# Performance work log

Hardware: AMD Instinct MI355X
Metric: run time of the kernel (lower is better)

The kernel has to match this reference:

```python
import jax, jax.numpy as jnp
import numpy as np

D_MODEL = 1024
NHEAD = 16
HEAD_DIM = D_MODEL // NHEAD


def setup_inputs() -> dict:
    key = jax.random.key(0)
    ks = jax.random.split(key, 11)
    B, S = 2, 2048
    s = 1.0 / np.sqrt(D_MODEL)
    return {
        "query": jax.random.normal(ks[0], (B, S, D_MODEL), jnp.float32),
        "key": jax.random.normal(ks[1], (B, S, D_MODEL), jnp.float32),
        "value": jax.random.normal(ks[2], (B, S, D_MODEL), jnp.float32),
        "wq_w": jax.random.normal(ks[3], (D_MODEL, D_MODEL), jnp.float32) * s,
        "wq_b": jax.random.normal(ks[4], (D_MODEL,), jnp.float32) * s,
        "wk_w": jax.random.normal(ks[5], (D_MODEL, D_MODEL), jnp.float32) * s,
        "wk_b": jax.random.normal(ks[6], (D_MODEL,), jnp.float32) * s,
        "wv_w": jax.random.normal(ks[7], (D_MODEL, D_MODEL), jnp.float32) * s,
        "wv_b": jax.random.normal(ks[8], (D_MODEL,), jnp.float32) * s,
        "wo_w": jax.random.normal(ks[9], (D_MODEL, D_MODEL), jnp.float32) * s,
        "wo_b": jax.random.normal(ks[10], (D_MODEL,), jnp.float32) * s,
    }


def reference(query, key, value, wq_w, wq_b, wk_w, wk_b, wv_w, wv_b, wo_w, wo_b):
    B, S, _ = query.shape
    # torch Linear: x @ W.T + b
    def proj(x, w, b):
        y = x @ w.T + b
        return y.reshape(B, S, NHEAD, HEAD_DIM).transpose(0, 2, 1, 3)  # [B,H,S,Dh]

    Q = proj(query, wq_w, wq_b)
    K = proj(key, wk_w, wk_b)
    V = proj(value, wv_w, wv_b)

    scale = 1.0 / np.sqrt(HEAD_DIM).astype(np.float32)
    scores = jnp.einsum("bhqd,bhkd->bhqk", Q, K) * scale  # [B,H,S,S]
    causal = jnp.tril(jnp.ones((S, S), dtype=bool))
    scores = jnp.where(causal, scores, -jnp.inf)
    attn = jax.nn.softmax(scores, axis=-1)
    out = jnp.einsum("bhqk,bhkd->bhqd", attn, V)  # [B,H,S,Dh]
    out = out.transpose(0, 2, 1, 3).reshape(B, S, D_MODEL)
    return out @ wo_w.T + wo_b
```

## Files before the change

### kernel.cpp

```cpp
#include <hip/hip_runtime.h>
#include <stdint.h>

#define D_MODEL 1024
#define S_LEN   2048
#define NHEAD   16
#define HEAD_DIM 64
#define BATCH   2
#define M_TOT   (BATCH * S_LEN)
#define Q_SCALE 0.18033688011112042f

using bf16x8 = __attribute__((ext_vector_type(8))) short;
using f32x4  = __attribute__((ext_vector_type(4))) float;

__device__ __forceinline__ unsigned short f2bf(float f) {
  union { float f; unsigned int u; } v; v.f = f;
  unsigned int u = v.u;
  return (unsigned short)((u + 0x7FFFu + ((u >> 16) & 1u)) >> 16);
}
__device__ __forceinline__ unsigned int pkbf(float a, float b) {
#if __has_builtin(__builtin_amdgcn_cvt_pk_bf16_f32)
  auto p = __builtin_amdgcn_cvt_pk_bf16_f32(a, b);
  union { decltype(p) v; unsigned int u; } c; c.v = p;
  return c.u;
#else
  return (unsigned int)f2bf(a) | ((unsigned int)f2bf(b) << 16);
#endif
}
__device__ __forceinline__ bf16x8 cvt8(const float* p) {
  const float4 a = *(const float4*)p;
  const float4 b = *(const float4*)(p + 4);
  union { unsigned int u[4]; bf16x8 v; } r;
  r.u[0] = pkbf(a.x, a.y); r.u[1] = pkbf(a.z, a.w);
  r.u[2] = pkbf(b.x, b.y); r.u[3] = pkbf(b.z, b.w);
  return r.v;
}
__device__ __forceinline__ float fexp2(float x) {
#if __has_builtin(__builtin_amdgcn_exp2f)
  return __builtin_amdgcn_exp2f(x);
#else
  return __expf(x * 0.69314718055994531f);
#endif
}
__device__ __forceinline__ void async16(const unsigned short* g, short* l) {
  __builtin_amdgcn_global_load_lds(
      reinterpret_cast<const __attribute__((address_space(1))) unsigned int*>(
          reinterpret_cast<uintptr_t>(g)),
      reinterpret_cast<__attribute__((address_space(3))) unsigned int*>(
          reinterpret_cast<uintptr_t>(l)),
      16, 0, 0);
}

#define LDK 40

__global__ __launch_bounds__(256)
void cast_all(const float* __restrict__ wq, const float* __restrict__ wk,
              const float* __restrict__ wv, const float* __restrict__ wo,
              const float* __restrict__ q, const float* __restrict__ k,
              const float* __restrict__ v,
              unsigned short* __restrict__ wb,
              unsigned short* __restrict__ qb, unsigned short* __restrict__ kb,
              unsigned short* __restrict__ vb)
{
  const int z = blockIdx.y;
  const float* src;
  unsigned short* d;
  size_t n;
  switch (z) {
    case 0: src = wq; d = wb;                                   n = (size_t)D_MODEL * D_MODEL; break;
    case 1: src = wk; d = wb + (size_t)1 * D_MODEL * D_MODEL;   n = (size_t)D_MODEL * D_MODEL; break;
    case 2: src = wv; d = wb + (size_t)2 * D_MODEL * D_MODEL;   n = (size_t)D_MODEL * D_MODEL; break;
    case 3: src = wo; d = wb + (size_t)3 * D_MODEL * D_MODEL;   n = (size_t)D_MODEL * D_MODEL; break;
    case 4: src = q;  d = qb;                                   n = (size_t)M_TOT * D_MODEL;   break;
    case 5: src = k;  d = kb;                                   n = (size_t)M_TOT * D_MODEL;   break;
    default: src = v; d = vb;                                   n = (size_t)M_TOT * D_MODEL;   break;
  }
  const size_t i = ((size_t)blockIdx.x * 256 + threadIdx.x) * 8;
  if (i < n) *(bf16x8*)(d + i) = cvt8(src + i);
}

__device__ __forceinline__ void gemm_tile_lds(const unsigned short* __restrict__ A,
                                              const unsigned short* __restrict__ W,
                                              int m0, int n0,
                                              short* As, short* Bs,
                                              f32x4 acc[4][4])
{
  const int t    = threadIdx.x;
  const int lane = t & 63;
  const int w    = t >> 6;
  const int quad = lane >> 4;
  const int l16  = lane & 15;
  const int wm   = (w >> 1) * 64;
  const int wn   = (w & 1) * 64;
  const int srow = w * 16 + (lane >> 2);
  const int scol = (lane & 3) * 8;

  for (int mt = 0; mt < 4; ++mt)
    for (int nt = 0; nt < 4; ++nt)
      acc[mt][nt] = f32x4{0.f, 0.f, 0.f, 0.f};

  for (int kt = 0; kt < D_MODEL / 32; ++kt) {
    const int kc = kt * 32 + scol;
    __syncthreads();
    async16(A + (size_t)(m0 + srow)      * D_MODEL + kc, As + srow * 32 + scol);
    async16(A + (size_t)(m0 + 64 + srow) * D_MODEL + kc, As + (64 + srow) * 32 + scol);
    async16(W + (size_t)(n0 + srow)      * D_MODEL + kc, Bs + srow * 32 + scol);
    async16(W + (size_t)(n0 + 64 + srow) * D_MODEL + kc, Bs + (64 + srow) * 32 + scol);
    __syncthreads();

    bf16x8 af[4], bfr[4];
    for (int mt = 0; mt < 4; ++mt)
      af[mt] = *(const bf16x8*)(As + (wm + mt * 16 + l16) * 32 + quad * 8);
    for (int nt = 0; nt < 4; ++nt)
      bfr[nt] = *(const bf16x8*)(Bs + (wn + nt * 16 + l16) * 32 + quad * 8);
    for (int mt = 0; mt < 4; ++mt)
      for (int nt = 0; nt < 4; ++nt)
        acc[mt][nt] = __builtin_amdgcn_mfma_f32_16x16x32_bf16(af[mt], bfr[nt], acc[mt][nt], 0, 0, 0);
  }
}

__device__ __forceinline__ void gemm_tile_f32(const float* __restrict__ A,
                                              const unsigned short* __restrict__ W,
                                              int m0, int n0,
                                              short* As, short* Bs,
                                              f32x4 acc[4][4])
{
  const int t    = threadIdx.x;
  const int lane = t & 63;
  const int w    = t >> 6;
  const int quad = lane >> 4;
  const int l16  = lane & 15;
  const int wm   = (w >> 1) * 64;
  const int wn   = (w & 1) * 64;
  const int srow = t >> 2;
  const int scol = (t & 3) * 8;

  for (int mt = 0; mt < 4; ++mt)
    for (int nt = 0; nt < 4; ++nt)
      acc[mt][nt] = f32x4{0.f, 0.f, 0.f, 0.f};

  for (int kt = 0; kt < D_MODEL / 32; ++kt) {
    const int kc = kt * 32 + scol;
    const bf16x8 a0 = cvt8(A + (size_t)(m0 + srow)      * D_MODEL + kc);
    const bf16x8 a1 = cvt8(A + (size_t)(m0 + srow + 64) * D_MODEL + kc);
    const bf16x8 b0 = *(const bf16x8*)(W + (size_t)(n0 + srow)      * D_MODEL + kc);
    const bf16x8 b1 = *(const bf16x8*)(W + (size_t)(n0 + srow + 64) * D_MODEL + kc);
    __syncthreads();
    *(bf16x8*)(As + (srow)      * LDK + scol) = a0;
    *(bf16x8*)(As + (srow + 64) * LDK + scol) = a1;
    *(bf16x8*)(Bs + (srow)      * LDK + scol) = b0;
    *(bf16x8*)(Bs + (srow + 64) * LDK + scol) = b1;
    __syncthreads();

    bf16x8 af[4], bfr[4];
    for (int mt = 0; mt < 4; ++mt)
      af[mt] = *(const bf16x8*)(As + (wm + mt * 16 + l16) * LDK + quad * 8);
    for (int nt = 0; nt < 4; ++nt)
      bfr[nt] = *(const bf16x8*)(Bs + (wn + nt * 16 + l16) * LDK + quad * 8);
    for (int mt = 0; mt < 4; ++mt)
      for (int nt = 0; nt < 4; ++nt)
        acc[mt][nt] = __builtin_amdgcn_mfma_f32_16x16x32_bf16(af[mt], bfr[nt], acc[mt][nt], 0, 0, 0);
  }
}

__device__ __forceinline__ void qkv_epilogue(int z, int m0, int n0,
                                             const float* __restrict__ bias,
                                             float scale,
                                             unsigned short* __restrict__ dst,
                                             f32x4 acc[4][4])
{
  const int t    = threadIdx.x;
  const int lane = t & 63;
  const int w    = t >> 6;
  const int quad = lane >> 4;
  const int l16  = lane & 15;
  const int wm   = (w >> 1) * 64;
  const int wn   = (w & 1) * 64;

  for (int nt = 0; nt < 4; ++nt) {
    const int n = n0 + wn + nt * 16 + l16;
    const float bb = bias[n];
    const int h = n >> 6, d = n & 63;
    for (int mt = 0; mt < 4; ++mt) {
      for (int r = 0; r < 4; ++r) {
        const int m = m0 + wm + mt * 16 + quad * 4 + r;
        const int b = m >> 11, s = m & 2047;
        const unsigned short val = f2bf((acc[mt][nt][r] + bb) * scale);
        if (z < 2)
          dst[((size_t)((b * NHEAD + h) * S_LEN + s)) * HEAD_DIM + d] = val;
        else
          dst[((size_t)((b * NHEAD + h) * HEAD_DIM + d)) * S_LEN + s] = val;
      }
    }
  }
}

__global__ __launch_bounds__(256)
void qkv_fast(const unsigned short* __restrict__ qb,
              const unsigned short* __restrict__ kb,
              const unsigned short* __restrict__ vb,
              const unsigned short* __restrict__ wqb,
              const unsigned short* __restrict__ wkb,
              const unsigned short* __restrict__ wvb,
              const float* __restrict__ bq, const float* __restrict__ bk,
              const float* __restrict__ bv,
              unsigned short* __restrict__ Qh, unsigned short* __restrict__ Kh,
              unsigned short* __restrict__ VhT)
{
  __shared__ __attribute__((aligned(16))) short As[128 * 32];
  __shared__ __attribute__((aligned(16))) short Bs[128 * 32];
  const int z = blockIdx.z;
  const unsigned short* A    = (z == 0) ? qb  : (z == 1) ? kb  : vb;
  const unsigned short* W    = (z == 0) ? wqb : (z == 1) ? wkb : wvb;
  const float*          bias = (z == 0) ? bq  : (z == 1) ? bk  : bv;
  unsigned short*       dst  = (z == 0) ? Qh  : (z == 1) ? Kh  : VhT;
  const float           scale = (z == 0) ? Q_SCALE : 1.0f;

  const int m0 = blockIdx.x * 128, n0 = blockIdx.y * 128;
  f32x4 acc[4][4];
  gemm_tile_lds(A, W, m0, n0, As, Bs, acc);
  qkv_epilogue(z, m0, n0, bias, scale, dst, acc);
}

__global__ __launch_bounds__(256)
void qkv_slow(const float* __restrict__ query, const float* __restrict__ key,
              const float* __restrict__ value,
              const unsigned short* __restrict__ wqb,
              const unsigned short* __restrict__ wkb,
              const unsigned short* __restrict__ wvb,
              const float* __restrict__ bq, const float* __restrict__ bk,
              const float* __restrict__ bv,
              unsigned short* __restrict__ Qh, unsigned short* __restrict__ Kh,
              unsigned short* __restrict__ VhT)
{
  __shared__ __attribute__((aligned(16))) short As[128 * LDK];
  __shared__ __attribute__((aligned(16))) short Bs[128 * LDK];
  const int z = blockIdx.z;
  const float*          A    = (z == 0) ? query : (z == 1) ? key : value;
  const unsigned short* W    = (z == 0) ? wqb   : (z == 1) ? wkb : wvb;
  const float*          bias = (z == 0) ? bq    : (z == 1) ? bk  : bv;
  unsigned short*       dst  = (z == 0) ? Qh    : (z == 1) ? Kh  : VhT;
  const float           scale = (z == 0) ? Q_SCALE : 1.0f;

  const int m0 = blockIdx.x * 128, n0 = blockIdx.y * 128;
  f32x4 acc[4][4];
  gemm_tile_f32(A, W, m0, n0, As, Bs, acc);
  qkv_epilogue(z, m0, n0, bias, scale, dst, acc);
}

__global__ __launch_bounds__(256)
void out_proj(const unsigned short* __restrict__ Oh,
              const unsigned short* __restrict__ wob,
              const float* __restrict__ bo,
              float* __restrict__ dst)
{
  __shared__ __attribute__((aligned(16))) short As[128 * 32];
  __shared__ __attribute__((aligned(16))) short Bs[128 * 32];
  const int m0 = blockIdx.x * 128, n0 = blockIdx.y * 128;
  f32x4 acc[4][4];
  gemm_tile_lds(Oh, wob, m0, n0, As, Bs, acc);

  const int t    = threadIdx.x;
  const int lane = t & 63;
  const int w    = t >> 6;
  const int quad = lane >> 4;
  const int l16  = lane & 15;
  const int wm   = (w >> 1) * 64;
  const int wn   = (w & 1) * 64;

  for (int nt = 0; nt < 4; ++nt) {
    const int n = n0 + wn + nt * 16 + l16;
    const float bb = bo[n];
    for (int mt = 0; mt < 4; ++mt)
      for (int r = 0; r < 4; ++r) {
        const int m = m0 + wm + mt * 16 + quad * 4 + r;
        dst[(size_t)m * D_MODEL + n] = acc[mt][nt][r] + bb;
      }
  }
}

__global__ __launch_bounds__(256)
void attn_kernel(const unsigned short* __restrict__ Qh,
                 const unsigned short* __restrict__ Kh,
                 const unsigned short* __restrict__ VhT,
                 unsigned short* __restrict__ O)
{
  __shared__ __attribute__((aligned(16))) short Ks[128 * 72];
  __shared__ __attribute__((aligned(16))) short Vts[64 * 136];
  __shared__ __attribute__((aligned(16))) short Ps[4][16 * 136];

  const int bh   = blockIdx.x;
  const int qt   = (int)gridDim.y - 1 - (int)blockIdx.y;
  const int q0   = qt * 64;
  const int b    = bh >> 4;
  const int h    = bh & 15;
  const int t    = threadIdx.x;
  const int w    = t >> 6;
  const int lane = t & 63;
  const int quad = lane >> 4;
  const int l16  = lane & 15;
  const size_t headK = (size_t)bh * S_LEN * HEAD_DIM;
  const size_t headV = (size_t)bh * HEAD_DIM * S_LEN;

  bf16x8 qf[2];
  {
    const size_t qrow = (size_t)bh * S_LEN + (q0 + w * 16 + l16);
    qf[0] = *(const bf16x8*)(Qh + qrow * HEAD_DIM + quad * 8);
    qf[1] = *(const bf16x8*)(Qh + qrow * HEAD_DIM + 32 + quad * 8);
  }
  bf16x8 ones;
  for (int j = 0; j < 8; ++j) ones[j] = (short)0x3F80;

  f32x4 lacc = f32x4{0.f, 0.f, 0.f, 0.f};
  f32x4 oacc[4];
  for (int dt = 0; dt < 4; ++dt) oacc[dt] = f32x4{0.f, 0.f, 0.f, 0.f};

  const int rowbase = q0 + w * 16;
  const int rowmax  = rowbase + 15;
  const int kr = t >> 3, kc = (t & 7) * 8;
  const int vd = t >> 4, vc = (t & 15) * 8;

  const int nkt = (qt + 2) >> 1;
  for (int kt = 0; kt < nkt; ++kt) {
    const int k0 = kt * 128;
    __syncthreads();
    for (int i = 0; i < 4; ++i) {
      const int rr = kr + i * 32;
      *(bf16x8*)(Ks + rr * 72 + kc) =
          *(const bf16x8*)(Kh + headK + (size_t)(k0 + rr) * HEAD_DIM + kc);
      const int dd = vd + i * 16;
      *(bf16x8*)(Vts + dd * 136 + vc) =
          *(const bf16x8*)(VhT + headV + (size_t)dd * S_LEN + k0 + vc);
    }
    __syncthreads();

    float st[8][4];
    for (int nt = 0; nt < 8; ++nt) {
      const int c0 = k0 + nt * 16;
      if (c0 <= rowmax) {
        f32x4 s = f32x4{0.f, 0.f, 0.f, 0.f};
        for (int ks = 0; ks < 2; ++ks) {
          const bf16x8 kf = *(const bf16x8*)(Ks + (nt * 16 + l16) * 72 + ks * 32 + quad * 8);
          s = __builtin_amdgcn_mfma_f32_16x16x32_bf16(qf[ks], kf, s, 0, 0, 0);
        }
        if (c0 + 15 <= rowbase) {
          for (int r = 0; r < 4; ++r) st[nt][r] = fexp2(s[r]);
        } else {
          const int colg = c0 + l16;
          for (int r = 0; r < 4; ++r) {
            const int rowg = rowbase + quad * 4 + r;
            st[nt][r] = (colg <= rowg) ? fexp2(s[r]) : 0.f;
          }
        }
      } else {
        for (int r = 0; r < 4; ++r) st[nt][r] = 0.f;
      }
    }
    for (int nt = 0; nt < 8; nt += 2) {
      for (int r = 0; r < 4; ++r) {
        const unsigned int u = pkbf(st[nt][r], st[nt + 1][r]);
        short* base = &Ps[w][(quad * 4 + r) * 136 + nt * 16 + l16];
        base[0]  = (short)(u & 0xffffu);
        base[16] = (short)(u >> 16);
      }
    }

    for (int ks = 0; ks < 4; ++ks) {
      if (k0 + ks * 32 > rowmax) break;
      const bf16x8 pf = *(const bf16x8*)(&Ps[w][0] + l16 * 136 + ks * 32 + quad * 8);
      lacc = __builtin_amdgcn_mfma_f32_16x16x32_bf16(pf, ones, lacc, 0, 0, 0);
      for (int dt = 0; dt < 4; ++dt) {
        const bf16x8 vf = *(const bf16x8*)(Vts + (dt * 16 + l16) * 136 + ks * 32 + quad * 8);
        oacc[dt] = __builtin_amdgcn_mfma_f32_16x16x32_bf16(pf, vf, oacc[dt], 0, 0, 0);
      }
    }
  }

  for (int dt = 0; dt < 4; ++dt) {
    for (int r = 0; r < 4; ++r) {
      const int rowg = q0 + w * 16 + quad * 4 + r;
      O[(size_t)(b * S_LEN + rowg) * D_MODEL + h * 64 + dt * 16 + l16] =
          f2bf(oacc[dt][r] / lacc[r]);
    }
  }
}

extern "C" void kernel_launch(void* const* d_in, const int* in_sizes, int n_in,
                              void* d_out, int out_size, void* d_ws, size_t ws_size,
                              hipStream_t stream)
{
  (void)in_sizes; (void)n_in; (void)out_size;
  const float* q  = (const float*)d_in[0];
  const float* k  = (const float*)d_in[1];
  const float* v  = (const float*)d_in[2];
  const float* wq = (const float*)d_in[3];
  const float* bq = (const float*)d_in[4];
  const float* wk = (const float*)d_in[5];
  const float* bk = (const float*)d_in[6];
  const float* wv = (const float*)d_in[7];
  const float* bv = (const float*)d_in[8];
  const float* wo = (const float*)d_in[9];
  const float* bo = (const float*)d_in[10];
  float* out = (float*)d_out;

  unsigned short* wb  = (unsigned short*)d_ws;
  unsigned short* wqb = wb;
  unsigned short* wkb = wb + (size_t)1 * D_MODEL * D_MODEL;
  unsigned short* wvb = wb + (size_t)2 * D_MODEL * D_MODEL;
  unsigned short* wob = wb + (size_t)3 * D_MODEL * D_MODEL;
  unsigned short* Kh  = wb + (size_t)4 * D_MODEL * D_MODEL;
  unsigned short* VhT = Kh + (size_t)M_TOT * D_MODEL;
  unsigned short* Oh  = VhT + (size_t)M_TOT * D_MODEL;
  unsigned short* qb  = Oh;
  unsigned short* vb  = Oh + (size_t)M_TOT * D_MODEL;
  unsigned short* Qh  = (unsigned short*)d_out;
  unsigned short* kb  = Qh + (size_t)M_TOT * D_MODEL;

  const bool fast = ws_size >= (size_t)40 * 1024 * 1024;

  dim3 g1(M_TOT / 128, D_MODEL / 128, 3);
  if (fast) {
    dim3 gc((size_t)M_TOT * D_MODEL / (256 * 8), 7, 1);
    cast_all<<<gc, 256, 0, stream>>>(wq, wk, wv, wo, q, k, v, wb, qb, kb, vb);
    qkv_fast<<<g1, 256, 0, stream>>>(qb, kb, vb, wqb, wkb, wvb, bq, bk, bv, Qh, Kh, VhT);
  } else {
    dim3 gc((size_t)D_MODEL * D_MODEL / (256 * 8), 4, 1);
    cast_all<<<gc, 256, 0, stream>>>(wq, wk, wv, wo, q, k, v, wb, qb, kb, vb);
    qkv_slow<<<g1, 256, 0, stream>>>(q, k, v, wqb, wkb, wvb, bq, bk, bv, Qh, Kh, VhT);
  }

  dim3 g2(BATCH * NHEAD, S_LEN / 64, 1);
  attn_kernel<<<g2, 256, 0, stream>>>(Qh, Kh, VhT, Oh);

  dim3 g3(M_TOT / 128, D_MODEL / 128, 1);
  out_proj<<<g3, 256, 0, stream>>>(Oh, wob, bo, out);
}
```

Measured before the change: 223.5 us.

## Keep attention probabilities in registers via transposed QK^T and permlane swaps

```diff
diff --git a/kernel.cpp b/kernel.cpp
--- a/kernel.cpp
+++ b/kernel.cpp
@@ -48,6 +48,33 @@
       reinterpret_cast<__attribute__((address_space(3))) unsigned int*>(
           reinterpret_cast<uintptr_t>(l)),
       16, 0, 0);
+}
+
+__device__ __forceinline__ void swap32(unsigned int& x, unsigned int& y) {
+#if __has_builtin(__builtin_amdgcn_permlane32_swap)
+  auto r = __builtin_amdgcn_permlane32_swap(x, y, false, false);
+  x = (unsigned int)r[0]; y = (unsigned int)r[1];
+#else
+  const int lane = threadIdx.x & 63;
+  unsigned int sx = (unsigned int)__shfl_xor((int)x, 32);
+  unsigned int sy = (unsigned int)__shfl_xor((int)y, 32);
+  unsigned int nx = (lane & 32) ? sy : x;
+  unsigned int ny = (lane & 32) ? y : sx;
+  x = nx; y = ny;
+#endif
+}
+__device__ __forceinline__ void swap16(unsigned int& x, unsigned int& y) {
+#if __has_builtin(__builtin_amdgcn_permlane16_swap)
+  auto r = __builtin_amdgcn_permlane16_swap(x, y, false, false);
+  x = (unsigned int)r[0]; y = (unsigned int)r[1];
+#else
+  const int lane = threadIdx.x & 63;
+  unsigned int sx = (unsigned int)__shfl_xor((int)x, 16);
+  unsigned int sy = (unsigned int)__shfl_xor((int)y, 16);
+  unsigned int nx = (lane & 16) ? sy : x;
+  unsigned int ny = (lane & 16) ? y : sx;
+  x = nx; y = ny;
+#endif
 }
 
 #define LDK 40
@@ -257,7 +284,7 @@
   __shared__ __attribute__((aligned(16))) short Bs[128 * 32];
   const int m0 = blockIdx.x * 128, n0 = blockIdx.y * 128;
   f32x4 acc[4][4];
-  gemm_tile_lds(Oh, wob, m0, n0, As, Bs, acc);
+  gemm_tile_lds(Oh, wob, bo ? m0 : m0, n0, As, Bs, acc);
 
   const int t    = threadIdx.x;
   const int lane = t & 63;
@@ -286,7 +313,6 @@
 {
   __shared__ __attribute__((aligned(16))) short Ks[128 * 72];
   __shared__ __attribute__((aligned(16))) short Vts[64 * 136];
-  __shared__ __attribute__((aligned(16))) short Ps[4][16 * 136];
 
   const int bh   = blockIdx.x;
   const int qt   = (int)gridDim.y - 1 - (int)blockIdx.y;
@@ -316,6 +342,7 @@
 
   const int rowbase = q0 + w * 16;
   const int rowmax  = rowbase + 15;
+  const int qg      = rowbase + l16;
   const int kr = t >> 3, kc = (t & 7) * 8;
   const int vd = t >> 4, vc = (t & 15) * 8;
 
@@ -334,43 +361,48 @@
     __syncthreads();
 
     float st[8][4];
+#pragma unroll
     for (int nt = 0; nt < 8; ++nt) {
       const int c0 = k0 + nt * 16;
       if (c0 <= rowmax) {
         f32x4 s = f32x4{0.f, 0.f, 0.f, 0.f};
+#pragma unroll
         for (int ks = 0; ks < 2; ++ks) {
           const bf16x8 kf = *(const bf16x8*)(Ks + (nt * 16 + l16) * 72 + ks * 32 + quad * 8);
-          s = __builtin_amdgcn_mfma_f32_16x16x32_bf16(qf[ks], kf, s, 0, 0, 0);
+          s = __builtin_amdgcn_mfma_f32_16x16x32_bf16(kf, qf[ks], s, 0, 0, 0);
         }
         if (c0 + 15 <= rowbase) {
+#pragma unroll
           for (int r = 0; r < 4; ++r) st[nt][r] = fexp2(s[r]);
         } else {
-          const int colg = c0 + l16;
-          for (int r = 0; r < 4; ++r) {
-            const int rowg = rowbase + quad * 4 + r;
-            st[nt][r] = (colg <= rowg) ? fexp2(s[r]) : 0.f;
-          }
+          const int kgb = c0 + quad * 4;
+#pragma unroll
+          for (int r = 0; r < 4; ++r)
+            st[nt][r] = (kgb + r <= qg) ? fexp2(s[r]) : 0.f;
         }
       } else {
+#pragma unroll
         for (int r = 0; r < 4; ++r) st[nt][r] = 0.f;
       }
     }
-    for (int nt = 0; nt < 8; nt += 2) {
-      for (int r = 0; r < 4; ++r) {
-        const unsigned int u = pkbf(st[nt][r], st[nt + 1][r]);
-        short* base = &Ps[w][(quad * 4 + r) * 136 + nt * 16 + l16];
-        base[0]  = (short)(u & 0xffffu);
-        base[16] = (short)(u >> 16);
-      }
-    }
-
+
+#pragma unroll
     for (int ks = 0; ks < 4; ++ks) {
-      if (k0 + ks * 32 > rowmax) break;
-      const bf16x8 pf = *(const bf16x8*)(&Ps[w][0] + l16 * 136 + ks * 32 + quad * 8);
-      lacc = __builtin_amdgcn_mfma_f32_16x16x32_bf16(pf, ones, lacc, 0, 0, 0);
-      for (int dt = 0; dt < 4; ++dt) {
-        const bf16x8 vf = *(const bf16x8*)(Vts + (dt * 16 + l16) * 136 + ks * 32 + quad * 8);
-        oacc[dt] = __builtin_amdgcn_mfma_f32_16x16x32_bf16(pf, vf, oacc[dt], 0, 0, 0);
+      if (k0 + ks * 32 <= rowmax) {
+        unsigned int pa = pkbf(st[2 * ks][0],     st[2 * ks][1]);
+        unsigned int pb = pkbf(st[2 * ks][2],     st[2 * ks][3]);
+        unsigned int pc = pkbf(st[2 * ks + 1][0], st[2 * ks + 1][1]);
+        unsigned int pe = pkbf(st[2 * ks + 1][2], st[2 * ks + 1][3]);
+        swap32(pa, pc); swap32(pb, pe);
+        swap16(pa, pc); swap16(pb, pe);
+        union { unsigned int u[4]; bf16x8 v; } pf;
+        pf.u[0] = pa; pf.u[1] = pb; pf.u[2] = pc; pf.u[3] = pe;
+        lacc = __builtin_amdgcn_mfma_f32_16x16x32_bf16(pf.v, ones, lacc, 0, 0, 0);
+#pragma unroll
+        for (int dt = 0; dt < 4; ++dt) {
+          const bf16x8 vf = *(const bf16x8*)(Vts + (dt * 16 + l16) * 136 + ks * 32 + quad * 8);
+          oacc[dt] = __builtin_amdgcn_mfma_f32_16x16x32_bf16(pf.v, vf, oacc[dt], 0, 0, 0);
+        }
       }
     }
   }
```

Result: faster. 217.8 us (-2.5%).
